# Performance work log

Measured on AMD Instinct MI355X. Metric: run time of the kernel, lower is better.

Reference implementation:

```python
import jax, jax.numpy as jnp
import numpy as np

N_ANCHORS = 250000
NUM_CLASSES = 80
K = 2048            # fixed NMS candidate capacity (static-shape stand-in for boolean filter)
CONF_TH = 0.05
IOU_TH = 0.5


def setup_inputs() -> dict:
    key = jax.random.key(0)
    k1, k2, k3, k4 = jax.random.split(key, 4)
    cls_logits = jax.random.normal(k1, (1, N_ANCHORS, NUM_CLASSES), dtype=jnp.float32)
    centerness = jax.random.normal(k2, (1, N_ANCHORS), dtype=jnp.float32)
    # well-formed xyxy boxes in a ~1024px canvas (bbox_reg is used directly as boxes in NMS)
    xy = jax.random.uniform(k3, (1, N_ANCHORS, 2), dtype=jnp.float32) * 1024.0
    wh = jax.random.uniform(k4, (1, N_ANCHORS, 2), dtype=jnp.float32) * 128.0 + 4.0
    bbox_reg = jnp.concatenate([xy, xy + wh], axis=-1)
    return {"cls_logits": cls_logits, "bbox_reg": bbox_reg, "centerness": centerness}


def _iou_matrix(b):
    # b: [K,4] xyxy -> [K,K] pairwise IoU
    x1, y1, x2, y2 = b[:, 0], b[:, 1], b[:, 2], b[:, 3]
    area = (x2 - x1) * (y2 - y1)
    xx1 = jnp.maximum(x1[:, None], x1[None, :])
    yy1 = jnp.maximum(y1[:, None], y1[None, :])
    xx2 = jnp.minimum(x2[:, None], x2[None, :])
    yy2 = jnp.minimum(y2[:, None], y2[None, :])
    inter = jnp.maximum(xx2 - xx1, 0.0) * jnp.maximum(yy2 - yy1, 0.0)
    union = area[:, None] + area[None, :] - inter
    return inter / jnp.maximum(union, 1e-9)


def reference(cls_logits, bbox_reg, centerness):
    B, N, C = cls_logits.shape
    cls_probs = jax.nn.sigmoid(cls_logits)                 # [B,N,C]
    center_probs = jax.nn.sigmoid(centerness)              # [B,N]
    scores = cls_probs * center_probs[..., None]           # [B,N,C]
    max_scores = jnp.max(scores, axis=-1).reshape(-1)      # [B*N]
    labels = jnp.argmax(scores, axis=-1).reshape(-1)       # [B*N]
    scores = scores.reshape(-1, C)
    boxes = bbox_reg.reshape(-1, 4)

    # confidence filter realized as masked top-K (static shapes)
    masked = jnp.where(max_scores > CONF_TH, max_scores, -jnp.inf)
    top_scores, idx = jax.lax.top_k(masked, K)
    valid = jnp.isfinite(top_scores)                       # [K]
    boxes_k = boxes[idx]                                   # [K,4] sorted by score desc
    labels_k = labels[idx]
    scores_k = scores[idx]
    ms_k = max_scores[idx]

    # batched (class-wise) NMS: offset boxes per class so classes never suppress each other
    max_coord = jnp.max(jnp.where(valid[:, None], boxes_k, 0.0))
    off = labels_k.astype(boxes_k.dtype) * (max_coord + 1.0)
    iou = _iou_matrix(boxes_k + off[:, None])              # [K,K]

    rng = jnp.arange(K)

    def body(i, keep):
        sup = (iou[i] > IOU_TH) & (rng > i) & keep[i]
        return keep & ~sup

    keep = jax.lax.fori_loop(0, K, body, valid)            # [K] bool
    return boxes_k, scores_k, ms_k, labels_k.astype(jnp.int32), keep
```

## Files before the change

kernel.cpp:

```cpp
#include <hip/hip_runtime.h>
#include <stdint.h>

#define NA 250000
#define NC 80
#define KSEL 2048
#define CONF_THF 0.05f
#define IOU_THF 0.5f
#define HBINS 1024
#define HREP 16
#define HBASE 0x3D00u
#define EMAX 4096u
#define K5BLK 64

typedef unsigned int u32;
typedef unsigned long long u64;

#define WS_HIST    0u
#define WS_SCAL    65536u
#define WS_VBITS   65600u
#define WS_RANK    65856u
#define WS_MAXS    82240u
#define WS_LABELS  1082240u
#define WS_CAND    2082240u
#define WS_SIDX    2098624u
#define WS_VALID   2106816u
#define WS_EDGES   2115008u

__device__ __forceinline__ float sigmoidf_(float x) {
  if (x >= 0.0f) {
    float ef = (float)exp(-(double)x);
    return 1.0f / (1.0f + ef);
  } else {
    float ef = (float)exp((double)x);
    return ef / (1.0f + ef);
  }
}

__device__ __forceinline__ float sigmoid_fast(float x) {
  return 1.0f / (1.0f + __expf(-x));
}

__device__ __forceinline__ u64 cand_key(const float* __restrict__ maxs,
                                        const u32* __restrict__ cand, u32 i) {
  u32 a = cand[i];
  float s = maxs[a];
  u32 kb = (s > CONF_THF) ? __float_as_uint(s) : 0u;
  return ((u64)kb << 32) | (u64)(0xFFFFFFFFu - a);
}

__global__ void __launch_bounds__(256)
k1_scores(const float* __restrict__ cls, const float* __restrict__ cent,
          float* __restrict__ maxs, int* __restrict__ labels) {
  int t = blockIdx.x * 256 + threadIdx.x;
  int a = t >> 2, p = t & 3;
  if (a >= NA) return;
  const float4* row = (const float4*)(cls + (size_t)a * NC) + p * 5;
  float4 r0 = row[0], r1 = row[1], r2 = row[2], r3 = row[3], r4 = row[4];

  float lm = fmaxf(fmaxf(fmaxf(r0.x, r0.y), fmaxf(r0.z, r0.w)),
                   fmaxf(fmaxf(r1.x, r1.y), fmaxf(r1.z, r1.w)));
  lm = fmaxf(lm, fmaxf(fmaxf(r2.x, r2.y), fmaxf(r2.z, r2.w)));
  lm = fmaxf(lm, fmaxf(fmaxf(r3.x, r3.y), fmaxf(r3.z, r3.w)));
  lm = fmaxf(lm, fmaxf(fmaxf(r4.x, r4.y), fmaxf(r4.z, r4.w)));
  lm = fmaxf(lm, __shfl_xor(lm, 1));
  lm = fmaxf(lm, __shfl_xor(lm, 2));

  float cv = 0.0f;
  if (p == 0) cv = cent[a];
  float xin = (p == 0) ? cv : lm;
  float sg = 0.0f;
  if (p < 2) sg = sigmoidf_(xin);
  int qb = (threadIdx.x & 63) & ~3;
  float cp   = __shfl(sg, qb);
  float slm  = __shfl(sg, qb + 1);
  float smax = slm * cp;

  float thresh = lm - 2e-4f;
  int firstEq = 0x7fffffff;
  int wcnt = 0;
  {
    float vv[20] = {r0.x, r0.y, r0.z, r0.w, r1.x, r1.y, r1.z, r1.w,
                    r2.x, r2.y, r2.z, r2.w, r3.x, r3.y, r3.z, r3.w,
                    r4.x, r4.y, r4.z, r4.w};
#pragma unroll
    for (int q = 0; q < 20; q++) {
      int c = p * 20 + q;
      if (vv[q] == lm && c < firstEq) firstEq = c;
      wcnt += (vv[q] >= thresh) ? 1 : 0;
    }
#pragma unroll
    for (int off = 1; off <= 2; off <<= 1) {
      int oe = __shfl_xor(firstEq, off);
      int ow = __shfl_xor(wcnt, off);
      firstEq = (oe < firstEq) ? oe : firstEq;
      wcnt += ow;
    }
    float bs; int bc;
    if (wcnt <= 1) {
      bs = smax;
      bc = firstEq;
    } else {
      bs = -1.0f; bc = 0x7fffffff;
#pragma unroll
      for (int q = 0; q < 20; q++) {
        if (vv[q] >= thresh) {
          float s = sigmoidf_(vv[q]) * cp;
          int c = p * 20 + q;
          if (s > bs || (s == bs && c < bc)) { bs = s; bc = c; }
        }
      }
#pragma unroll
      for (int off = 1; off <= 2; off <<= 1) {
        float os = __shfl_xor(bs, off);
        int   oc = __shfl_xor(bc, off);
        if (os > bs || (os == bs && oc < bc)) { bs = os; bc = oc; }
      }
    }
    if (p == 0) {
      maxs[a] = bs;
      labels[a] = bc;
    }
  }
}

__global__ void __launch_bounds__(1024) kH_hist(const float* __restrict__ maxs,
                                                u32* __restrict__ hist) {
  __shared__ u32 lh[HBINS];
  for (int i = threadIdx.x; i < HBINS; i += 1024) lh[i] = 0u;
  __syncthreads();
  for (u32 a = blockIdx.x * 1024 + threadIdx.x; a < NA; a += 16 * 1024) {
    float s = maxs[a];
    if (s > CONF_THF) {
      u32 bin = (__float_as_uint(s) >> 16) - HBASE;
      atomicAdd(&lh[bin], 1u);
    }
  }
  __syncthreads();
  for (int i = threadIdx.x; i < HBINS; i += 1024)
    hist[(blockIdx.x << 10) + i] = lh[i];
}

__global__ void __launch_bounds__(1024) k2_findbin(const u32* __restrict__ hist,
                                                   u32* __restrict__ scal,
                                                   u32* __restrict__ vbits32,
                                                   u32* __restrict__ rankArr) {
  __shared__ u32 sc[1024];
  int tid = threadIdx.x;
  if (tid < 16) scal[tid] = 0u;
  if (tid < 64) vbits32[tid] = 0u;
#pragma unroll
  for (int i = 0; i < 4; i++) rankArr[tid + i * 1024] = 0u;

  int bin = 1023 - tid;
  u32 c = 0;
#pragma unroll
  for (int r = 0; r < HREP; r++) c += hist[r * HBINS + bin];
  sc[tid] = c;
  for (int off = 1; off < 1024; off <<= 1) {
    __syncthreads();
    u32 t = (tid >= off) ? sc[tid - off] : 0u;
    __syncthreads();
    sc[tid] += t;
  }
  __syncthreads();
  u32 incl = sc[tid], excl = incl - c;
  if (incl >= KSEL && excl < KSEL) {
    scal[2] = ((u32)bin + HBASE) << 16;
    scal[1] = excl;
  }
  if (tid == 1023 && incl < KSEL) {
    scal[2] = 0u;
    scal[1] = incl;
  }
}

__global__ void __launch_bounds__(1024) k5_compact(const float* __restrict__ maxs,
                                                   u32* __restrict__ scal,
                                                   u32* __restrict__ cand) {
  __shared__ u32 lcnt, lbase;
  __shared__ u32 llist[1024];
  if (threadIdx.x == 0) lcnt = 0u;
  __syncthreads();
  u32 kth = scal[2];
  for (u32 a = blockIdx.x * 1024 + threadIdx.x; a < NA; a += K5BLK * 1024) {
    float s = maxs[a];
    u32 key = (s > CONF_THF) ? __float_as_uint(s) : 0u;
    if (key >= kth && (key > 0u || a < KSEL)) {
      u32 p = atomicAdd(&lcnt, 1u);
      if (p < 1024u) llist[p] = a;
    }
  }
  __syncthreads();
  u32 n = lcnt < 1024u ? lcnt : 1024u;
  if (threadIdx.x == 0) lbase = atomicAdd(&scal[3], n);
  __syncthreads();
  u32 base = lbase;
  for (u32 j = threadIdx.x; j < n; j += 1024) {
    u32 pos = base + j;
    if (pos < 4096u) cand[pos] = llist[j];
  }
}

__global__ void __launch_bounds__(256) k6a_rank(const float* __restrict__ maxs,
                                                const u32* __restrict__ cand,
                                                const u32* __restrict__ scal,
                                                u32* __restrict__ rankArr) {
  __shared__ u64 keys[256];
  u32 cnt = scal[3];
  u32 nn = cnt < 4096u ? cnt : 4096u;
  u32 seg0 = blockIdx.y * 256;
  u32 cg0 = blockIdx.x * 256;
  if (seg0 >= nn || cg0 >= nn) return;
  int tid = threadIdx.x;
  u32 si = seg0 + tid;
  keys[tid] = (si < nn) ? cand_key(maxs, cand, si) : 0ull;
  __syncthreads();
  u32 ci = cg0 + tid;
  if (ci >= nn) return;
  u64 mykey = cand_key(maxs, cand, ci);
  u32 lim = nn - seg0; if (lim > 256u) lim = 256u;
  u32 r = 0, i = 0;
  for (; i + 8 <= lim; i += 8) {
    r += (keys[i]     > mykey);
    r += (keys[i + 1] > mykey);
    r += (keys[i + 2] > mykey);
    r += (keys[i + 3] > mykey);
    r += (keys[i + 4] > mykey);
    r += (keys[i + 5] > mykey);
    r += (keys[i + 6] > mykey);
    r += (keys[i + 7] > mykey);
  }
  for (; i < lim; ++i) r += (keys[i] > mykey);
  if (r) atomicAdd(&rankArr[ci], r);
}

__global__ void __launch_bounds__(256) k6b_scatter(const float* __restrict__ maxs,
                                                   const u32* __restrict__ cand,
                                                   const u32* __restrict__ scal,
                                                   const u32* __restrict__ rankArr,
                                                   const float* __restrict__ bbox,
                                                   u32* __restrict__ sidx,
                                                   u32* __restrict__ validArr,
                                                   u32* __restrict__ validBits32,
                                                   u32* __restrict__ scalW) {
  u32 cnt = scal[3];
  u32 nn = cnt < 4096u ? cnt : 4096u;
  u32 ci = blockIdx.x * 256 + threadIdx.x;
  float m = -1.0f;
  if (ci < nn) {
    u64 mykey = cand_key(maxs, cand, ci);
    u32 rank = rankArr[ci];
    if (rank < KSEL) {
      u32 a = 0xFFFFFFFFu - (u32)(mykey & 0xFFFFFFFFu);
      bool valid = (mykey >> 32) != 0ull;
      sidx[rank] = a;
      validArr[rank] = valid ? 1u : 0u;
      if (valid) {
        atomicOr(&validBits32[rank >> 5], 1u << (rank & 31));
        float4 b4 = ((const float4*)bbox)[a];
        m = fmaxf(fmaxf(b4.x, b4.y), fmaxf(b4.z, b4.w));
      }
    }
  }
#pragma unroll
  for (int off = 1; off < 64; off <<= 1) m = fmaxf(m, __shfl_xor(m, off));
  if ((threadIdx.x & 63) == 0 && m >= 0.0f)
    atomicMax((int*)&scalW[4], __float_as_int(m));
}

__global__ void k7_gather(const float* __restrict__ cls, const float* __restrict__ cent,
                          const float* __restrict__ bbox, const float* __restrict__ maxs,
                          const int* __restrict__ labels, const u32* __restrict__ sidx,
                          float* __restrict__ out) {
  int r = blockIdx.x;
  int tid = threadIdx.x;
  u32 a = sidx[r];
  float* out_boxes  = out;
  float* out_scores = out + KSEL * 4;
  float* out_ms     = out + KSEL * 4 + KSEL * NC;
  float* out_lab    = out_ms + KSEL;
  if (tid < NC) {
    float cp = sigmoid_fast(cent[a]);
    float s = sigmoid_fast(cls[(size_t)a * NC + tid]) * cp;
    out_scores[(size_t)r * NC + tid] = s;
  } else if (tid < NC + 4) {
    int q = tid - NC;
    out_boxes[r * 4 + q] = bbox[(size_t)a * 4 + q];
  } else if (tid == NC + 4) {
    out_ms[r] = maxs[a];
  } else if (tid == NC + 5) {
    out_lab[r] = (float)labels[a];
  }
}

__global__ void k8_edges(const float* __restrict__ out, u32* __restrict__ scal,
                         u32* __restrict__ edges) {
  if (blockIdx.x < blockIdx.y) return;
  __shared__ float cx1[64], cy1[64], cx2[64], cy2[64], car[64];
  const float* boxes = out;
  const float* lab = out + KSEL * 4 + KSEL * NC + KSEL;
  float mc1 = __int_as_float(*(const int*)&scal[4]) + 1.0f;
  int t = threadIdx.x;
  int j0 = blockIdx.x * 64;
  int j = j0 + t;
  {
    float off = lab[j] * mc1;
    float x1 = boxes[j * 4 + 0] + off, y1 = boxes[j * 4 + 1] + off;
    float x2 = boxes[j * 4 + 2] + off, y2 = boxes[j * 4 + 3] + off;
    cx1[t] = x1; cy1[t] = y1; cx2[t] = x2; cy2[t] = y2;
    car[t] = (x2 - x1) * (y2 - y1);
  }
  __syncthreads();
  int i = blockIdx.y * 64 + t;
  float off = lab[i] * mc1;
  float x1 = boxes[i * 4 + 0] + off, y1 = boxes[i * 4 + 1] + off;
  float x2 = boxes[i * 4 + 2] + off, y2 = boxes[i * 4 + 3] + off;
  float ar = (x2 - x1) * (y2 - y1);
  for (int jj = 0; jj < 64; jj++) {
    float ix = fminf(x2, cx2[jj]) - fmaxf(x1, cx1[jj]);
    float iy = fminf(y2, cy2[jj]) - fmaxf(y1, cy1[jj]);
    float inter = fmaxf(ix, 0.0f) * fmaxf(iy, 0.0f);
    float uni = ar + car[jj] - inter;
    float iou = inter / fmaxf(uni, 1e-9f);
    int jidx = j0 + jj;
    if (iou > IOU_THF && i < jidx) {
      u32 pos = atomicAdd(&scal[5], 1u);
      if (pos < EMAX) edges[pos] = ((u32)i << 12) | (u32)jidx;
    }
  }
}

__global__ void k9_nms(const u32* __restrict__ edges, const u32* __restrict__ scal,
                       const u64* __restrict__ validBits,
                       float* __restrict__ out_keep) {
  __shared__ u32 aliveLds[64];
  __shared__ u32 supLds[64];
  int lane = threadIdx.x;
  u32 E = scal[5]; if (E > EMAX) E = EMAX;
  u64 vw = (lane < 32) ? validBits[lane] : 0ull;
  u64 alive = vw;
  for (int it = 0; it < 2048; ++it) {
    if (lane < 32) {
      aliveLds[2 * lane]     = (u32)alive;
      aliveLds[2 * lane + 1] = (u32)(alive >> 32);
    }
    supLds[lane] = 0u;
    __syncthreads();
    for (u32 e = lane; e < E; e += 64) {
      u32 p = edges[e];
      u32 i = p >> 12, j = p & 0xFFFu;
      if ((aliveLds[i >> 5] >> (i & 31)) & 1u)
        atomicOr(&supLds[j >> 5], 1u << (j & 31));
    }
    __syncthreads();
    u64 na = alive;
    if (lane < 32) {
      u64 sup = (u64)supLds[2 * lane] | ((u64)supLds[2 * lane + 1] << 32);
      na = vw & ~sup;
    }
    u64 anych = __ballot(na != alive);
    alive = na;
    __syncthreads();
    if (anych == 0ull) break;
  }
  if (lane < 32) {
    aliveLds[2 * lane]     = (u32)alive;
    aliveLds[2 * lane + 1] = (u32)(alive >> 32);
  }
  __syncthreads();
#pragma unroll
  for (int t = 0; t < 32; ++t) {
    int idx = t * 64 + lane;
    out_keep[idx] = ((aliveLds[idx >> 5] >> (idx & 31)) & 1u) ? 1.0f : 0.0f;
  }
}

extern "C" void kernel_launch(void* const* d_in, const int* in_sizes, int n_in,
                              void* d_out, int out_size, void* d_ws, size_t ws_size,
                              hipStream_t stream) {
  const float* cls  = (const float*)d_in[0];
  const float* bbox = (const float*)d_in[1];
  const float* cent = (const float*)d_in[2];
  float* out = (float*)d_out;
  char* ws = (char*)d_ws;
  u32* hist      = (u32*)(ws + WS_HIST);
  u32* scal      = (u32*)(ws + WS_SCAL);
  u32* vbits32   = (u32*)(ws + WS_VBITS);
  u32* rankArr   = (u32*)(ws + WS_RANK);
  float* maxs    = (float*)(ws + WS_MAXS);
  int* labels    = (int*)(ws + WS_LABELS);
  u32* cand      = (u32*)(ws + WS_CAND);
  u32* sidx      = (u32*)(ws + WS_SIDX);
  u32* validArr  = (u32*)(ws + WS_VALID);
  u32* edges     = (u32*)(ws + WS_EDGES);

  (void)in_sizes; (void)n_in; (void)out_size; (void)ws_size; (void)validArr;

  k1_scores<<<(NA * 4 + 255) / 256, 256, 0, stream>>>(cls, cent, maxs, labels);
  kH_hist<<<16, 1024, 0, stream>>>(maxs, hist);
  k2_findbin<<<1, 1024, 0, stream>>>(hist, scal, vbits32, rankArr);
  k5_compact<<<K5BLK, 1024, 0, stream>>>(maxs, scal, cand);
  k6a_rank<<<dim3(16, 16), 256, 0, stream>>>(maxs, cand, scal, rankArr);
  k6b_scatter<<<16, 256, 0, stream>>>(maxs, cand, scal, rankArr, bbox, sidx, validArr, vbits32, scal);
  k7_gather<<<KSEL, 128, 0, stream>>>(cls, cent, bbox, maxs, labels, sidx, out);
  k8_edges<<<dim3(32, 32), 64, 0, stream>>>(out, scal, edges);
  k9_nms<<<1, 64, 0, stream>>>(edges, scal, (const u64*)vbits32, out + KSEL * 4 + KSEL * NC + KSEL * 2);
}
```

Measured before the change: 62.03 us.

## Fuse gather into scatter, interleave class loads, and launch triangular edge grid

Removes the separate k7_gather kernel. The scatter kernel now writes boxes, max scores, labels and the full per-class sigmoid score row directly at each candidate's rank, so the sidx/validArr round trip goes away. k1 reads the class row in an interleaved float4 pattern so the four lanes of an anchor touch adjacent 16-byte chunks, with the class-index arithmetic remapped to match. k8_edges launches only the 528 upper-triangular tiles, decoding each tile from a linear block id, instead of a 32x32 grid with early exits. One drawback is that the 80-float score row is now written by a single thread in a 16-block kernel, which gives far less parallelism than the 2048-block gather it replaces.

```diff
diff --git a/kernel.cpp b/kernel.cpp
--- a/kernel.cpp
+++ b/kernel.cpp
@@ -22,8 +22,6 @@
 #define WS_MAXS    82240u
 #define WS_LABELS  1082240u
 #define WS_CAND    2082240u
-#define WS_SIDX    2098624u
-#define WS_VALID   2106816u
 #define WS_EDGES   2115008u
 
 __device__ __forceinline__ float sigmoidf_(float x) {
@@ -54,8 +52,9 @@
   int t = blockIdx.x * 256 + threadIdx.x;
   int a = t >> 2, p = t & 3;
   if (a >= NA) return;
-  const float4* row = (const float4*)(cls + (size_t)a * NC) + p * 5;
-  float4 r0 = row[0], r1 = row[1], r2 = row[2], r3 = row[3], r4 = row[4];
+  const float4* row = (const float4*)(cls + (size_t)a * NC);
+  float4 r0 = row[p], r1 = row[p + 4], r2 = row[p + 8],
+         r3 = row[p + 12], r4 = row[p + 16];
 
   float lm = fmaxf(fmaxf(fmaxf(r0.x, r0.y), fmaxf(r0.z, r0.w)),
                    fmaxf(fmaxf(r1.x, r1.y), fmaxf(r1.z, r1.w)));
@@ -83,10 +82,10 @@
                     r2.x, r2.y, r2.z, r2.w, r3.x, r3.y, r3.z, r3.w,
                     r4.x, r4.y, r4.z, r4.w};
 #pragma unroll
-    for (int q = 0; q < 20; q++) {
-      int c = p * 20 + q;
-      if (vv[q] == lm && c < firstEq) firstEq = c;
-      wcnt += (vv[q] >= thresh) ? 1 : 0;
+    for (int j = 0; j < 20; j++) {
+      int c = 16 * (j >> 2) + 4 * p + (j & 3);
+      if (vv[j] == lm && c < firstEq) firstEq = c;
+      wcnt += (vv[j] >= thresh) ? 1 : 0;
     }
 #pragma unroll
     for (int off = 1; off <= 2; off <<= 1) {
@@ -102,10 +101,10 @@
     } else {
       bs = -1.0f; bc = 0x7fffffff;
 #pragma unroll
-      for (int q = 0; q < 20; q++) {
-        if (vv[q] >= thresh) {
-          float s = sigmoidf_(vv[q]) * cp;
-          int c = p * 20 + q;
+      for (int j = 0; j < 20; j++) {
+        if (vv[j] >= thresh) {
+          float s = sigmoidf_(vv[j]) * cp;
+          int c = 16 * (j >> 2) + 4 * p + (j & 3);
           if (s > bs || (s == bs && c < bc)) { bs = s; bc = c; }
         }
       }
@@ -236,13 +235,18 @@
 
 __global__ void __launch_bounds__(256) k6b_scatter(const float* __restrict__ maxs,
                                                    const u32* __restrict__ cand,
-                                                   const u32* __restrict__ scal,
+                                                   u32* __restrict__ scal,
                                                    const u32* __restrict__ rankArr,
                                                    const float* __restrict__ bbox,
-                                                   u32* __restrict__ sidx,
-                                                   u32* __restrict__ validArr,
+                                                   const float* __restrict__ cls,
+                                                   const float* __restrict__ cent,
+                                                   const int* __restrict__ labels,
                                                    u32* __restrict__ validBits32,
-                                                   u32* __restrict__ scalW) {
+                                                   float* __restrict__ out) {
+  float* out_boxes  = out;
+  float* out_scores = out + KSEL * 4;
+  float* out_ms     = out + KSEL * 4 + KSEL * NC;
+  float* out_lab    = out_ms + KSEL;
   u32 cnt = scal[3];
   u32 nn = cnt < 4096u ? cnt : 4096u;
   u32 ci = blockIdx.x * 256 + threadIdx.x;
@@ -253,55 +257,49 @@
     if (rank < KSEL) {
       u32 a = 0xFFFFFFFFu - (u32)(mykey & 0xFFFFFFFFu);
       bool valid = (mykey >> 32) != 0ull;
-      sidx[rank] = a;
-      validArr[rank] = valid ? 1u : 0u;
+      float4 b4 = ((const float4*)bbox)[a];
+      ((float4*)out_boxes)[rank] = b4;
+      out_ms[rank] = maxs[a];
+      out_lab[rank] = (float)labels[a];
       if (valid) {
         atomicOr(&validBits32[rank >> 5], 1u << (rank & 31));
-        float4 b4 = ((const float4*)bbox)[a];
         m = fmaxf(fmaxf(b4.x, b4.y), fmaxf(b4.z, b4.w));
       }
+      float cp = sigmoid_fast(cent[a]);
+      const float4* crow = (const float4*)(cls + (size_t)a * NC);
+      float4* srow = (float4*)(out_scores + (size_t)rank * NC);
+#pragma unroll
+      for (int j = 0; j < 20; j++) {
+        float4 v = crow[j];
+        float4 s;
+        s.x = sigmoid_fast(v.x) * cp;
+        s.y = sigmoid_fast(v.y) * cp;
+        s.z = sigmoid_fast(v.z) * cp;
+        s.w = sigmoid_fast(v.w) * cp;
+        srow[j] = s;
+      }
     }
   }
 #pragma unroll
   for (int off = 1; off < 64; off <<= 1) m = fmaxf(m, __shfl_xor(m, off));
   if ((threadIdx.x & 63) == 0 && m >= 0.0f)
-    atomicMax((int*)&scalW[4], __float_as_int(m));
-}
-
-__global__ void k7_gather(const float* __restrict__ cls, const float* __restrict__ cent,
-                          const float* __restrict__ bbox, const float* __restrict__ maxs,
-                          const int* __restrict__ labels, const u32* __restrict__ sidx,
-                          float* __restrict__ out) {
-  int r = blockIdx.x;
-  int tid = threadIdx.x;
-  u32 a = sidx[r];
-  float* out_boxes  = out;
-  float* out_scores = out + KSEL * 4;
-  float* out_ms     = out + KSEL * 4 + KSEL * NC;
-  float* out_lab    = out_ms + KSEL;
-  if (tid < NC) {
-    float cp = sigmoid_fast(cent[a]);
-    float s = sigmoid_fast(cls[(size_t)a * NC + tid]) * cp;
-    out_scores[(size_t)r * NC + tid] = s;
-  } else if (tid < NC + 4) {
-    int q = tid - NC;
-    out_boxes[r * 4 + q] = bbox[(size_t)a * 4 + q];
-  } else if (tid == NC + 4) {
-    out_ms[r] = maxs[a];
-  } else if (tid == NC + 5) {
-    out_lab[r] = (float)labels[a];
-  }
-}
-
-__global__ void k8_edges(const float* __restrict__ out, u32* __restrict__ scal,
-                         u32* __restrict__ edges) {
-  if (blockIdx.x < blockIdx.y) return;
+    atomicMax((int*)&scal[4], __float_as_int(m));
+}
+
+__global__ void __launch_bounds__(64) k8_edges(const float* __restrict__ out,
+                                               u32* __restrict__ scal,
+                                               u32* __restrict__ edges) {
   __shared__ float cx1[64], cy1[64], cx2[64], cy2[64], car[64];
+  int bid = blockIdx.x;
+  int bx = (int)((sqrtf(8.0f * bid + 1.0f) - 1.0f) * 0.5f);
+  while ((bx + 1) * (bx + 2) / 2 <= bid) bx++;
+  while (bx * (bx + 1) / 2 > bid) bx--;
+  int by = bid - bx * (bx + 1) / 2;
   const float* boxes = out;
   const float* lab = out + KSEL * 4 + KSEL * NC + KSEL;
   float mc1 = __int_as_float(*(const int*)&scal[4]) + 1.0f;
   int t = threadIdx.x;
-  int j0 = blockIdx.x * 64;
+  int j0 = bx * 64;
   int j = j0 + t;
   {
     float off = lab[j] * mc1;
@@ -311,7 +309,7 @@
     car[t] = (x2 - x1) * (y2 - y1);
   }
   __syncthreads();
-  int i = blockIdx.y * 64 + t;
+  int i = by * 64 + t;
   float off = lab[i] * mc1;
   float x1 = boxes[i * 4 + 0] + off, y1 = boxes[i * 4 + 1] + off;
   float x2 = boxes[i * 4 + 2] + off, y2 = boxes[i * 4 + 3] + off;
@@ -390,19 +388,18 @@
   float* maxs    = (float*)(ws + WS_MAXS);
   int* labels    = (int*)(ws + WS_LABELS);
   u32* cand      = (u32*)(ws + WS_CAND);
-  u32* sidx      = (u32*)(ws + WS_SIDX);
-  u32* validArr  = (u32*)(ws + WS_VALID);
   u32* edges     = (u32*)(ws + WS_EDGES);
 
-  (void)in_sizes; (void)n_in; (void)out_size; (void)ws_size; (void)validArr;
+  (void)in_sizes; (void)n_in; (void)out_size; (void)ws_size;
 
   k1_scores<<<(NA * 4 + 255) / 256, 256, 0, stream>>>(cls, cent, maxs, labels);
   kH_hist<<<16, 1024, 0, stream>>>(maxs, hist);
   k2_findbin<<<1, 1024, 0, stream>>>(hist, scal, vbits32, rankArr);
   k5_compact<<<K5BLK, 1024, 0, stream>>>(maxs, scal, cand);
   k6a_rank<<<dim3(16, 16), 256, 0, stream>>>(maxs, cand, scal, rankArr);
-  k6b_scatter<<<16, 256, 0, stream>>>(maxs, cand, scal, rankArr, bbox, sidx, validArr, vbits32, scal);
-  k7_gather<<<KSEL, 128, 0, stream>>>(cls, cent, bbox, maxs, labels, sidx, out);
-  k8_edges<<<dim3(32, 32), 64, 0, stream>>>(out, scal, edges);
-  k9_nms<<<1, 64, 0, stream>>>(edges, scal, (const u64*)vbits32, out + KSEL * 4 + KSEL * NC + KSEL * 2);
-}
+  k6b_scatter<<<16, 256, 0, stream>>>(maxs, cand, scal, rankArr, bbox, cls, cent,
+                                      labels, vbits32, out);
+  k8_edges<<<528, 64, 0, stream>>>(out, scal, edges);
+  k9_nms<<<1, 64, 0, stream>>>(edges, scal, (const u64*)vbits32,
+                               out + KSEL * 4 + KSEL * NC + KSEL * 2);
+}
```

After: 65.88 us. 1.06x slower.

## Fold bin-finding scan into compaction kernel and move workspace zeroing into histogram

Applied to the files above, without the earlier changes.

Removes the separate single-block k2_findbin launch. Each k5_compact block now recomputes the histogram prefix scan itself and keeps the threshold bin in shared memory. Zeroing of scal, vbits32 and rankArr moves into block 0 of the histogram kernel. This cuts one kernel launch and its serialization gap on a short dependency chain, at the cost of 64 blocks repeating the small scan; scal[1] is no longer written, which matters only if a later kernel reads it.

```diff
diff --git a/kernel.cpp b/kernel.cpp
--- a/kernel.cpp
+++ b/kernel.cpp
@@ -124,11 +124,21 @@
 }
 
 __global__ void __launch_bounds__(1024) kH_hist(const float* __restrict__ maxs,
-                                                u32* __restrict__ hist) {
+                                                u32* __restrict__ hist,
+                                                u32* __restrict__ scal,
+                                                u32* __restrict__ vbits32,
+                                                u32* __restrict__ rankArr) {
   __shared__ u32 lh[HBINS];
-  for (int i = threadIdx.x; i < HBINS; i += 1024) lh[i] = 0u;
-  __syncthreads();
-  for (u32 a = blockIdx.x * 1024 + threadIdx.x; a < NA; a += 16 * 1024) {
+  int tid = threadIdx.x;
+  if (blockIdx.x == 0) {
+    if (tid < 16) scal[tid] = 0u;
+    if (tid < 64) vbits32[tid] = 0u;
+#pragma unroll
+    for (int i = 0; i < 4; i++) rankArr[tid + i * 1024] = 0u;
+  }
+  for (int i = tid; i < HBINS; i += 1024) lh[i] = 0u;
+  __syncthreads();
+  for (u32 a = blockIdx.x * 1024 + tid; a < NA; a += 16 * 1024) {
     float s = maxs[a];
     if (s > CONF_THF) {
       u32 bin = (__float_as_uint(s) >> 16) - HBASE;
@@ -136,21 +146,18 @@
     }
   }
   __syncthreads();
-  for (int i = threadIdx.x; i < HBINS; i += 1024)
+  for (int i = tid; i < HBINS; i += 1024)
     hist[(blockIdx.x << 10) + i] = lh[i];
 }
 
-__global__ void __launch_bounds__(1024) k2_findbin(const u32* __restrict__ hist,
+__global__ void __launch_bounds__(1024) k5_compact(const float* __restrict__ maxs,
+                                                   const u32* __restrict__ hist,
                                                    u32* __restrict__ scal,
-                                                   u32* __restrict__ vbits32,
-                                                   u32* __restrict__ rankArr) {
+                                                   u32* __restrict__ cand) {
   __shared__ u32 sc[1024];
+  __shared__ u32 llist[1024];
+  __shared__ u32 lcnt, lbase, kthS;
   int tid = threadIdx.x;
-  if (tid < 16) scal[tid] = 0u;
-  if (tid < 64) vbits32[tid] = 0u;
-#pragma unroll
-  for (int i = 0; i < 4; i++) rankArr[tid + i * 1024] = 0u;
-
   int bin = 1023 - tid;
   u32 c = 0;
 #pragma unroll
@@ -158,31 +165,18 @@
   sc[tid] = c;
   for (int off = 1; off < 1024; off <<= 1) {
     __syncthreads();
-    u32 t = (tid >= off) ? sc[tid - off] : 0u;
+    u32 t2 = (tid >= off) ? sc[tid - off] : 0u;
     __syncthreads();
-    sc[tid] += t;
+    sc[tid] += t2;
   }
   __syncthreads();
   u32 incl = sc[tid], excl = incl - c;
-  if (incl >= KSEL && excl < KSEL) {
-    scal[2] = ((u32)bin + HBASE) << 16;
-    scal[1] = excl;
-  }
-  if (tid == 1023 && incl < KSEL) {
-    scal[2] = 0u;
-    scal[1] = incl;
-  }
-}
-
-__global__ void __launch_bounds__(1024) k5_compact(const float* __restrict__ maxs,
-                                                   u32* __restrict__ scal,
-                                                   u32* __restrict__ cand) {
-  __shared__ u32 lcnt, lbase;
-  __shared__ u32 llist[1024];
-  if (threadIdx.x == 0) lcnt = 0u;
-  __syncthreads();
-  u32 kth = scal[2];
-  for (u32 a = blockIdx.x * 1024 + threadIdx.x; a < NA; a += K5BLK * 1024) {
+  if (incl >= KSEL && excl < KSEL) kthS = ((u32)bin + HBASE) << 16;
+  if (tid == 1023 && incl < KSEL) kthS = 0u;
+  if (tid == 0) lcnt = 0u;
+  __syncthreads();
+  u32 kth = kthS;
+  for (u32 a = blockIdx.x * 1024 + tid; a < NA; a += K5BLK * 1024) {
     float s = maxs[a];
     u32 key = (s > CONF_THF) ? __float_as_uint(s) : 0u;
     if (key >= kth && (key > 0u || a < KSEL)) {
@@ -192,10 +186,10 @@
   }
   __syncthreads();
   u32 n = lcnt < 1024u ? lcnt : 1024u;
-  if (threadIdx.x == 0) lbase = atomicAdd(&scal[3], n);
+  if (tid == 0) lbase = atomicAdd(&scal[3], n);
   __syncthreads();
   u32 base = lbase;
-  for (u32 j = threadIdx.x; j < n; j += 1024) {
+  for (u32 j = tid; j < n; j += 1024) {
     u32 pos = base + j;
     if (pos < 4096u) cand[pos] = llist[j];
   }
@@ -394,12 +388,11 @@
   u32* validArr  = (u32*)(ws + WS_VALID);
   u32* edges     = (u32*)(ws + WS_EDGES);
 
-  (void)in_sizes; (void)n_in; (void)out_size; (void)ws_size; (void)validArr;
+  (void)in_sizes; (void)n_in; (void)out_size; (void)ws_size;
 
   k1_scores<<<(NA * 4 + 255) / 256, 256, 0, stream>>>(cls, cent, maxs, labels);
-  kH_hist<<<16, 1024, 0, stream>>>(maxs, hist);
-  k2_findbin<<<1, 1024, 0, stream>>>(hist, scal, vbits32, rankArr);
-  k5_compact<<<K5BLK, 1024, 0, stream>>>(maxs, scal, cand);
+  kH_hist<<<16, 1024, 0, stream>>>(maxs, hist, scal, vbits32, rankArr);
+  k5_compact<<<K5BLK, 1024, 0, stream>>>(maxs, hist, scal, cand);
   k6a_rank<<<dim3(16, 16), 256, 0, stream>>>(maxs, cand, scal, rankArr);
   k6b_scatter<<<16, 256, 0, stream>>>(maxs, cand, scal, rankArr, bbox, sidx, validArr, vbits32, scal);
   k7_gather<<<KSEL, 128, 0, stream>>>(cls, cent, bbox, maxs, labels, sidx, out);
```

Measured after the change: 60.26 us. 2.9% less time.
